# Performance work log

Hardware: AMD Instinct MI355X
Metric: run time of the kernel (lower is better)

Reference implementation:

```python
import jax, jax.numpy as jnp
import numpy as np

N = 50000
E = 800000
IN, HID, OUT = 20, 64, 2
HEADS, HD = 4, 64
EPS = 1e-5


def setup_inputs() -> dict:
    key = jax.random.key(0)
    ks = jax.random.split(key, 24)
    rn = lambda k, shape, s=0.1: (jax.random.normal(k, shape, dtype=jnp.float32) * s)
    inp = {}
    inp['x'] = jax.random.normal(ks[0], (N, IN), dtype=jnp.float32)
    inp['edge_index'] = jax.random.randint(ks[1], (2, E), 0, N, dtype=jnp.int64)
    # SAGEConv1: lin_l (aggregated msgs, bias), lin_r (root, no bias)
    inp['Wl1'] = rn(ks[2], (IN, HID)); inp['Wr1'] = rn(ks[3], (IN, HID)); inp['b1'] = jnp.zeros((HID,), jnp.float32)
    inp['g1'] = jnp.ones((HID,), jnp.float32); inp['bt1'] = jnp.zeros((HID,), jnp.float32)
    # GATConv: W2 projects to heads*dim; att vectors per head; bias size HID (concat=False)
    inp['W2'] = rn(ks[4], (HID, HEADS * HD)); inp['att_src'] = rn(ks[5], (HEADS, HD)); inp['att_dst'] = rn(ks[6], (HEADS, HD)); inp['b2'] = jnp.zeros((HID,), jnp.float32)
    inp['g2'] = jnp.ones((HID,), jnp.float32); inp['bt2'] = jnp.zeros((HID,), jnp.float32)
    # SAGEConv3: hidden -> hidden//2
    inp['Wl3'] = rn(ks[7], (HID, HID // 2)); inp['Wr3'] = rn(ks[8], (HID, HID // 2)); inp['b3'] = jnp.zeros((HID // 2,), jnp.float32)
    inp['g3'] = jnp.ones((HID // 2,), jnp.float32); inp['bt3'] = jnp.zeros((HID // 2,), jnp.float32)
    # skip + classifier
    inp['Wskip'] = rn(ks[9], (IN, HID // 2)); inp['bskip'] = jnp.zeros((HID // 2,), jnp.float32)
    inp['Wc1'] = rn(ks[10], (HID // 2, 32)); inp['bc1'] = jnp.zeros((32,), jnp.float32)
    inp['Wc2'] = rn(ks[11], (32, OUT)); inp['bc2'] = jnp.zeros((OUT,), jnp.float32)
    return inp


def _bn_eval(h, g, b):
    # eval-mode BatchNorm with freshly initialized running stats (mean=0, var=1)
    return h * (g / jnp.sqrt(1.0 + EPS)) + b


def reference(x, edge_index, Wl1, Wr1, b1, g1, bt1, W2, att_src, att_dst, b2, g2, bt2,
              Wl3, Wr3, b3, g3, bt3, Wskip, bskip, Wc1, bc1, Wc2, bc2):
    src, dst = edge_index[0], edge_index[1]
    deg = jnp.clip(jax.ops.segment_sum(jnp.ones((E,), x.dtype), dst, num_segments=N), 1.0)

    def sage(h, Wl, Wr, b):
        agg = jax.ops.segment_sum(h[src], dst, num_segments=N) / deg[:, None]  # mean aggregation
        return agg @ Wl + h @ Wr + b

    def gat(h):
        hp = (h @ W2).reshape(N, HEADS, HD)                    # [N,H,D]
        a_s = jnp.einsum('nhd,hd->nh', hp, att_src)            # [N,H]
        a_d = jnp.einsum('nhd,hd->nh', hp, att_dst)
        e = jax.nn.leaky_relu(a_s[src] + a_d[dst], 0.2)        # [E,H]
        m = jax.ops.segment_max(e, dst, num_segments=N)        # segment softmax over incoming edges
        ex = jnp.exp(e - m[dst])
        denom = jax.ops.segment_sum(ex, dst, num_segments=N)
        alpha = ex / (denom[dst] + 1e-16)                      # [E,H]
        out = jax.ops.segment_sum(hp[src] * alpha[:, :, None], dst, num_segments=N)  # [N,H,D]
        return out.mean(axis=1) + b2                            # concat=False -> mean over heads

    identity = x @ Wskip + bskip
    h = jax.nn.relu(_bn_eval(sage(x, Wl1, Wr1, b1), g1, bt1))   # dropout inactive (eval)
    h = jax.nn.relu(_bn_eval(gat(h), g2, bt2))
    h = jax.nn.relu(_bn_eval(sage(h, Wl3, Wr3, b3), g3, bt3))
    h = h + identity
    logits = jax.nn.relu(h @ Wc1 + bc1) @ Wc2 + bc2
    return jax.nn.log_softmax(logits, axis=1)
```

## Files before the change

### kernel.cpp

```cpp
#include <hip/hip_runtime.h>
#include <hip/hip_fp16.h>
#include <math.h>

#define NN 50000
#define NE 800000
#define IN_F 20
#define HID 64
#define HEADS 4
#define HD 64
#define CH 32
#define C1 32
#define OUTC 2

__global__ void k_count(const int* __restrict__ dst, int* __restrict__ count){
  int e = blockIdx.x * 256 + threadIdx.x;
  if (e < NE) atomicAdd(&count[dst[e]], 1);
}

__global__ void k_scan_block(const int* __restrict__ in, int* __restrict__ out,
                             int* __restrict__ bsum, int n){
  __shared__ int tmp[256];
  int g = blockIdx.x * 256 + threadIdx.x;
  int v = (g < n) ? in[g] : 0;
  tmp[threadIdx.x] = v;
  __syncthreads();
  for (int o = 1; o < 256; o <<= 1) {
    int t = ((int)threadIdx.x >= o) ? tmp[threadIdx.x - o] : 0;
    __syncthreads();
    tmp[threadIdx.x] += t;
    __syncthreads();
  }
  if (g < n) out[g] = tmp[threadIdx.x] - v;
  if (bsum && threadIdx.x == 255) bsum[blockIdx.x] = tmp[255];
}

__global__ void k_add_off(int* __restrict__ rowptr, const int* __restrict__ bsum_ex, int n){
  int g = blockIdx.x * 256 + threadIdx.x;
  if (g < n) rowptr[g] += bsum_ex[g >> 8];
  if (g == 0) rowptr[NN] = NE;
}

__global__ void k_scatter(const int* __restrict__ src, const int* __restrict__ dst,
                          const int* __restrict__ rowptr, int* __restrict__ cnt2,
                          int2* __restrict__ colrow){
  int e = blockIdx.x * 256 + threadIdx.x;
  if (e >= NE) return;
  int d = dst[e];
  int p = rowptr[d] + atomicAdd(&cnt2[d], 1);
  colrow[p] = make_int2(src[e], d);
}

__global__ void k_prep(const float* __restrict__ x, const float* __restrict__ W2,
                       const float* __restrict__ att_src, const float* __restrict__ att_dst,
                       __half* __restrict__ xh, float* __restrict__ was,
                       float* __restrict__ wad, float* __restrict__ W2r){
  int i = blockIdx.x * 256 + threadIdx.x;
  if (i < NN * IN_F) xh[i] = __float2half(x[i]);
  if (i < 256 * 64) {
    int hk = i >> 6, d = i & 63;
    int h = hk >> 6, k = hk & 63;
    W2r[i] = W2[k * 256 + h * 64 + d];
  }
  if (i < 256) {
    int h = i >> 6, k = i & 63;
    float s = 0.f, dd = 0.f;
    for (int d = 0; d < 64; d++) {
      float w = W2[k * 256 + h * 64 + d];
      s  += w * att_src[h * 64 + d];
      dd += w * att_dst[h * 64 + d];
    }
    was[i] = s; wad[i] = dd;
  }
}

__global__ void k_aggx_gather(const int* __restrict__ rowptr, const int2* __restrict__ colrow,
                              const __half* __restrict__ xh, float* __restrict__ aggx){
  int idx = blockIdx.x * 256 + threadIdx.x;
  if (idx >= NN * IN_F) return;
  int n = idx / IN_F, k = idx - n * IN_F;
  int r0 = rowptr[n], r1 = rowptr[n + 1];
  float acc = 0.f;
  int j = r0;
  for (; j + 4 <= r1; j += 4) {
    int s0 = colrow[j].x, s1 = colrow[j+1].x, s2 = colrow[j+2].x, s3 = colrow[j+3].x;
    float v0 = __half2float(xh[s0 * IN_F + k]);
    float v1 = __half2float(xh[s1 * IN_F + k]);
    float v2 = __half2float(xh[s2 * IN_F + k]);
    float v3 = __half2float(xh[s3 * IN_F + k]);
    acc += (v0 + v1) + (v2 + v3);
  }
  for (; j < r1; j++) acc += __half2float(xh[colrow[j].x * IN_F + k]);
  aggx[idx] = acc;
}

__global__ void k_sage1(const float* __restrict__ x, const float* __restrict__ aggx,
                        const int* __restrict__ count,
                        const float* __restrict__ Wl, const float* __restrict__ Wr,
                        const float* __restrict__ b, const float* __restrict__ g,
                        const float* __restrict__ bt,
                        const float* __restrict__ was, const float* __restrict__ wad,
                        __half* __restrict__ h1h, float* __restrict__ a_s,
                        float* __restrict__ a_d){
  __shared__ float sWl[IN_F * HID], sWr[IN_F * HID], sWas[256], sWad[256];
  for (int i = threadIdx.x; i < IN_F * HID; i += 256) { sWl[i] = Wl[i]; sWr[i] = Wr[i]; }
  { int i = threadIdx.x; sWas[i] = was[i]; sWad[i] = wad[i]; }
  __syncthreads();
  int idx = blockIdx.x * 256 + threadIdx.x;
  if (idx >= NN * HID) return;
  int n = idx >> 6, j = idx & 63;
  float inv = 1.f / fmaxf((float)count[n], 1.f);
  const float* xr = x + n * IN_F;
  const float* ar = aggx + n * IN_F;
  float acc = b[j];
  #pragma unroll
  for (int k = 0; k < IN_F; k++)
    acc += (ar[k] * inv) * sWl[k * HID + j] + xr[k] * sWr[k * HID + j];
  acc = acc * (g[j] * rsqrtf(1.f + 1e-5f)) + bt[j];
  acc = fmaxf(acc, 0.f);
  h1h[idx] = __float2half(acc);
  #pragma unroll
  for (int h = 0; h < HEADS; h++) {
    float vs = acc * sWas[h * 64 + j];
    float vd = acc * sWad[h * 64 + j];
    #pragma unroll
    for (int o = 32; o > 0; o >>= 1) { vs += __shfl_down(vs, o); vd += __shfl_down(vd, o); }
    if (j == 0) { a_s[n * 4 + h] = vs; a_d[n * 4 + h] = vd; }
  }
}

__global__ void k_edgep(const int2* __restrict__ colrow,
                        const float4* __restrict__ a_s4, const float4* __restrict__ a_d4,
                        float4* __restrict__ pe4){
  int j = blockIdx.x * 256 + threadIdx.x;
  if (j >= NE) return;
  int2 cr = colrow[j];
  float4 as = a_s4[cr.x];
  float4 ad = a_d4[cr.y];
  float e0 = as.x + ad.x; e0 = e0 >= 0.f ? e0 : 0.2f * e0;
  float e1 = as.y + ad.y; e1 = e1 >= 0.f ? e1 : 0.2f * e1;
  float e2 = as.z + ad.z; e2 = e2 >= 0.f ? e2 : 0.2f * e2;
  float e3 = as.w + ad.w; e3 = e3 >= 0.f ? e3 : 0.2f * e3;
  pe4[j] = make_float4(__expf(e0), __expf(e1), __expf(e2), __expf(e3));
}

__global__ void k_gat_fused(const int* __restrict__ rowptr, const int2* __restrict__ colrow,
                            const float4* __restrict__ pe4,
                            const __half* __restrict__ h1h, __half* __restrict__ z){
  int wid = threadIdx.x >> 6;
  int lane = threadIdx.x & 63;
  int grp = lane >> 5;
  int idx = lane & 31;
  int n = blockIdx.x * 4 + wid;
  if (n >= NN) return;
  int r0 = rowptr[n], r1 = rowptr[n + 1];
  float l0 = 0.f, l1 = 0.f, l2 = 0.f, l3 = 0.f;
  float2 ac0 = {0,0}, ac1 = {0,0}, ac2 = {0,0}, ac3 = {0,0};
  int base = r0;
  for (; base + 8 <= r1; base += 8) {
    int j0 = base + grp, j1 = base + 2 + grp, j2 = base + 4 + grp, j3 = base + 6 + grp;
    int s0 = colrow[j0].x, s1 = colrow[j1].x, s2 = colrow[j2].x, s3 = colrow[j3].x;
    float4 p0 = pe4[j0], p1 = pe4[j1], p2 = pe4[j2], p3 = pe4[j3];
    float2 v0 = __half22float2(*(const __half2*)(h1h + (size_t)s0 * 64 + 2 * idx));
    float2 v1 = __half22float2(*(const __half2*)(h1h + (size_t)s1 * 64 + 2 * idx));
    float2 v2 = __half22float2(*(const __half2*)(h1h + (size_t)s2 * 64 + 2 * idx));
    float2 v3 = __half22float2(*(const __half2*)(h1h + (size_t)s3 * 64 + 2 * idx));
    l0 += (p0.x + p1.x) + (p2.x + p3.x);
    l1 += (p0.y + p1.y) + (p2.y + p3.y);
    l2 += (p0.z + p1.z) + (p2.z + p3.z);
    l3 += (p0.w + p1.w) + (p2.w + p3.w);
    ac0.x += p0.x*v0.x + p1.x*v1.x + p2.x*v2.x + p3.x*v3.x;
    ac0.y += p0.x*v0.y + p1.x*v1.y + p2.x*v2.y + p3.x*v3.y;
    ac1.x += p0.y*v0.x + p1.y*v1.x + p2.y*v2.x + p3.y*v3.x;
    ac1.y += p0.y*v0.y + p1.y*v1.y + p2.y*v2.y + p3.y*v3.y;
    ac2.x += p0.z*v0.x + p1.z*v1.x + p2.z*v2.x + p3.z*v3.x;
    ac2.y += p0.z*v0.y + p1.z*v1.y + p2.z*v2.y + p3.z*v3.y;
    ac3.x += p0.w*v0.x + p1.w*v1.x + p2.w*v2.x + p3.w*v3.x;
    ac3.y += p0.w*v0.y + p1.w*v1.y + p2.w*v2.y + p3.w*v3.y;
  }
  for (int j = base + grp; j < r1; j += 2) {
    int s = colrow[j].x;
    float4 p = pe4[j];
    float2 v = __half22float2(*(const __half2*)(h1h + (size_t)s * 64 + 2 * idx));
    l0 += p.x; l1 += p.y; l2 += p.z; l3 += p.w;
    ac0.x += p.x*v.x; ac0.y += p.x*v.y;
    ac1.x += p.y*v.x; ac1.y += p.y*v.y;
    ac2.x += p.z*v.x; ac2.y += p.z*v.y;
    ac3.x += p.w*v.x; ac3.y += p.w*v.y;
  }
  l0 += __shfl_xor(l0, 32); l1 += __shfl_xor(l1, 32);
  l2 += __shfl_xor(l2, 32); l3 += __shfl_xor(l3, 32);
  ac0.x += __shfl_xor(ac0.x, 32); ac0.y += __shfl_xor(ac0.y, 32);
  ac1.x += __shfl_xor(ac1.x, 32); ac1.y += __shfl_xor(ac1.y, 32);
  ac2.x += __shfl_xor(ac2.x, 32); ac2.y += __shfl_xor(ac2.y, 32);
  ac3.x += __shfl_xor(ac3.x, 32); ac3.y += __shfl_xor(ac3.y, 32);
  if (grp == 0) {
    float i0 = 1.f / (4.f * (l0 + 1e-16f));
    float i1 = 1.f / (4.f * (l1 + 1e-16f));
    float i2 = 1.f / (4.f * (l2 + 1e-16f));
    float i3 = 1.f / (4.f * (l3 + 1e-16f));
    __half* zr = z + (size_t)n * 256;
    *(__half2*)(zr +       2 * idx) = __floats2half2_rn(ac0.x * i0, ac0.y * i0);
    *(__half2*)(zr +  64 + 2 * idx) = __floats2half2_rn(ac1.x * i1, ac1.y * i1);
    *(__half2*)(zr + 128 + 2 * idx) = __floats2half2_rn(ac2.x * i2, ac2.y * i2);
    *(__half2*)(zr + 192 + 2 * idx) = __floats2half2_rn(ac3.x * i3, ac3.y * i3);
  }
}

__global__ void __launch_bounds__(256) k_zproj(const __half* __restrict__ z,
                      const float* __restrict__ W2r, const float* __restrict__ b2,
                      const float* __restrict__ g2, const float* __restrict__ bt2,
                      float* __restrict__ h2, __half* __restrict__ h2h){
  __shared__ float sz[4][256];
  __shared__ float sacc[4][4][64];
  int tid = threadIdx.x;
  int w = tid >> 6, d = tid & 63;
  float wreg[64];
  #pragma unroll
  for (int i = 0; i < 64; i++) wreg[i] = W2r[(w * 64 + i) * 64 + d];
  float gd = g2[d] * rsqrtf(1.f + 1e-5f), btd = bt2[d], bd = b2[d];
  int n0base = blockIdx.x * 64;
  for (int r = 0; r < 16; r++) {
    int n0 = n0base + r * 4;
    for (int i = tid; i < 512; i += 256) {
      int m = i >> 7, c = (i & 127) * 2;
      int n = n0 + m;
      if (n < NN) {
        __half2 hv = *(const __half2*)(z + (size_t)n * 256 + c);
        float2 f = __half22float2(hv);
        sz[m][c] = f.x; sz[m][c + 1] = f.y;
      } else { sz[m][c] = 0.f; sz[m][c + 1] = 0.f; }
    }
    __syncthreads();
    #pragma unroll
    for (int m = 0; m < 4; m++) {
      float acc = 0.f;
      #pragma unroll
      for (int i = 0; i < 64; i++) acc += sz[m][w * 64 + i] * wreg[i];
      sacc[m][w][d] = acc;
    }
    __syncthreads();
    int n = n0 + w;
    if (n < NN) {
      float rr = sacc[w][0][d] + sacc[w][1][d] + sacc[w][2][d] + sacc[w][3][d] + bd;
      rr = rr * gd + btd;
      rr = fmaxf(rr, 0.f);
      h2[(size_t)n * 64 + d] = rr;
      h2h[(size_t)n * 64 + d] = __float2half(rr);
    }
    __syncthreads();
  }
}

__global__ void __launch_bounds__(256) k_sage3f(
    const int* __restrict__ rowptr, const int2* __restrict__ colrow,
    const float* __restrict__ x, const float* __restrict__ h2,
    const __half* __restrict__ h2h, const int* __restrict__ count,
    const float* __restrict__ Wl3, const float* __restrict__ Wr3,
    const float* __restrict__ b3, const float* __restrict__ g3,
    const float* __restrict__ bt3, const float* __restrict__ Wskip,
    const float* __restrict__ bskip, float* __restrict__ h3){
  __shared__ float sWl[HID * CH], sWr[HID * CH], sWs[IN_F * CH];
  __shared__ float sA[4][HID], sH[4][HID];
  for (int i = threadIdx.x; i < HID * CH; i += 256) { sWl[i] = Wl3[i]; sWr[i] = Wr3[i]; }
  for (int i = threadIdx.x; i < IN_F * CH; i += 256) sWs[i] = Wskip[i];
  int wid = threadIdx.x >> 6, lane = threadIdx.x & 63;
  int grp = lane >> 5, idx = lane & 31;
  int n = blockIdx.x * 4 + wid;
  int nc = n < NN ? n : NN - 1;
  int r0 = rowptr[nc], r1 = rowptr[nc + 1];
  float2 av = {0, 0};
  int base = r0;
  for (; base + 8 <= r1; base += 8) {
    int j0 = base + grp, j1 = base + 2 + grp, j2 = base + 4 + grp, j3 = base + 6 + grp;
    int s0 = colrow[j0].x, s1 = colrow[j1].x, s2 = colrow[j2].x, s3 = colrow[j3].x;
    float2 v0 = __half22float2(*(const __half2*)(h2h + (size_t)s0 * 64 + 2 * idx));
    float2 v1 = __half22float2(*(const __half2*)(h2h + (size_t)s1 * 64 + 2 * idx));
    float2 v2 = __half22float2(*(const __half2*)(h2h + (size_t)s2 * 64 + 2 * idx));
    float2 v3 = __half22float2(*(const __half2*)(h2h + (size_t)s3 * 64 + 2 * idx));
    av.x += (v0.x + v1.x) + (v2.x + v3.x);
    av.y += (v0.y + v1.y) + (v2.y + v3.y);
  }
  for (int j = base + grp; j < r1; j += 2) {
    float2 v = __half22float2(*(const __half2*)(h2h + (size_t)colrow[j].x * 64 + 2 * idx));
    av.x += v.x; av.y += v.y;
  }
  av.x += __shfl_xor(av.x, 32);
  av.y += __shfl_xor(av.y, 32);
  float inv = 1.f / fmaxf((float)count[nc], 1.f);
  if (grp == 0) { sA[wid][2 * idx] = av.x * inv; sA[wid][2 * idx + 1] = av.y * inv; }
  sH[wid][lane] = h2[(size_t)nc * 64 + lane];
  __syncthreads();
  int kbase = grp * 32;
  float c0 = 0.f, c1 = 0.f;
  #pragma unroll
  for (int k0 = 0; k0 < 32; k0 += 2) {
    int k = kbase + k0;
    c0 += sA[wid][k] * sWl[k * CH + idx] + sH[wid][k] * sWr[k * CH + idx];
    c1 += sA[wid][k+1] * sWl[(k+1) * CH + idx] + sH[wid][k+1] * sWr[(k+1) * CH + idx];
  }
  float c = c0 + c1;
  c += __shfl_xor(c, 32);
  if (grp == 0 && n < NN) {
    float acc = c + b3[idx];
    acc = acc * (g3[idx] * rsqrtf(1.f + 1e-5f)) + bt3[idx];
    acc = fmaxf(acc, 0.f);
    float idn = bskip[idx];
    const float* xr = x + (size_t)n * IN_F;
    #pragma unroll
    for (int k = 0; k < IN_F; k++) idn += xr[k] * sWs[k * CH + idx];
    h3[(size_t)n * CH + idx] = acc + idn;
  }
}

__global__ void __launch_bounds__(64) k_cls(const float* __restrict__ h3,
                      const float* __restrict__ Wc1, const float* __restrict__ bc1,
                      const float* __restrict__ Wc2, const float* __restrict__ bc2,
                      float* __restrict__ out){
  __shared__ float sW1[C1 * C1], sW2[C1 * OUTC], sb1[C1], sb2[OUTC];
  __shared__ float sh3[64][CH + 1];
  int tid = threadIdx.x;
  int n0 = blockIdx.x * 64;
  for (int i = tid; i < C1 * C1; i += 64) sW1[i] = Wc1[i];
  if (tid < C1 * OUTC) sW2[tid] = Wc2[tid];
  if (tid < C1) sb1[tid] = bc1[tid];
  if (tid < OUTC) sb2[tid] = bc2[tid];
  for (int i = tid; i < 64 * CH; i += 64) {
    int m = i >> 5, c = i & 31;
    int n = n0 + m;
    sh3[m][c] = (n < NN) ? h3[(size_t)n * CH + c] : 0.f;
  }
  __syncthreads();
  int n = n0 + tid;
  if (n >= NN) return;
  float hrow[CH];
  #pragma unroll
  for (int j = 0; j < CH; j++) hrow[j] = sh3[tid][j];
  float l0 = sb2[0], l1 = sb2[1];
  #pragma unroll
  for (int i = 0; i < C1; i++) {
    float c0 = sb1[i], c1 = 0.f;
    #pragma unroll
    for (int j = 0; j < CH; j += 2) {
      c0 += hrow[j] * sW1[j * C1 + i];
      c1 += hrow[j + 1] * sW1[(j + 1) * C1 + i];
    }
    float c = fmaxf(c0 + c1, 0.f);
    l0 += c * sW2[i * OUTC + 0];
    l1 += c * sW2[i * OUTC + 1];
  }
  float mx = fmaxf(l0, l1);
  float lse = mx + logf(expf(l0 - mx) + expf(l1 - mx));
  out[n * OUTC + 0] = l0 - lse;
  out[n * OUTC + 1] = l1 - lse;
}

extern "C" void kernel_launch(void* const* d_in, const int* in_sizes, int n_in,
                              void* d_out, int out_size, void* d_ws, size_t ws_size,
                              hipStream_t stream) {
  const float* x       = (const float*)d_in[0];
  const int*   ei      = (const int*)d_in[1];
  const float* Wl1     = (const float*)d_in[2];
  const float* Wr1     = (const float*)d_in[3];
  const float* b1      = (const float*)d_in[4];
  const float* g1      = (const float*)d_in[5];
  const float* bt1     = (const float*)d_in[6];
  const float* W2      = (const float*)d_in[7];
  const float* att_src = (const float*)d_in[8];
  const float* att_dst = (const float*)d_in[9];
  const float* b2      = (const float*)d_in[10];
  const float* g2      = (const float*)d_in[11];
  const float* bt2     = (const float*)d_in[12];
  const float* Wl3     = (const float*)d_in[13];
  const float* Wr3     = (const float*)d_in[14];
  const float* b3      = (const float*)d_in[15];
  const float* g3      = (const float*)d_in[16];
  const float* bt3     = (const float*)d_in[17];
  const float* Wskip   = (const float*)d_in[18];
  const float* bskip   = (const float*)d_in[19];
  const float* Wc1     = (const float*)d_in[20];
  const float* bc1     = (const float*)d_in[21];
  const float* Wc2     = (const float*)d_in[22];
  const float* bc2     = (const float*)d_in[23];
  float* out = (float*)d_out;

  const int* src = ei;
  const int* dst = ei + NE;

  float* ws = (float*)d_ws;
  size_t off = 0;
  auto alloc = [&](size_t nf) { size_t o = off; off += (nf + 63) & ~(size_t)63; return o; };
  size_t o_count = alloc(NN);
  size_t o_cnt2  = alloc(NN);
  size_t zero_elems = off;
  size_t o_rowptr = alloc(NN + 1);
  size_t o_bsum   = alloc(256);
  size_t o_bsumex = alloc(256);
  size_t o_colrow = alloc((size_t)NE * 2);
  size_t o_pe     = alloc((size_t)NE * 4);
  size_t o_xh     = alloc((size_t)NN * IN_F / 2 + 64);
  size_t o_aggx   = alloc((size_t)NN * IN_F);
  size_t o_h1h    = alloc((size_t)NN * HID / 2 + 64);
  size_t o_as     = alloc((size_t)NN * HEADS);
  size_t o_ad     = alloc((size_t)NN * HEADS);
  size_t o_was    = alloc(256);
  size_t o_wad    = alloc(256);
  size_t o_w2r    = alloc(256 * 64);
  size_t o_z      = alloc((size_t)NN * 256 / 2 + 64);
  size_t o_h2     = alloc((size_t)NN * HID);
  size_t o_h2h    = alloc((size_t)NN * HID / 2 + 64);
  size_t o_h3     = alloc((size_t)NN * CH);
  (void)ws_size; (void)in_sizes; (void)n_in; (void)out_size;

  int* count    = (int*)(ws + o_count);
  int* cnt2     = (int*)(ws + o_cnt2);
  int* rowptr   = (int*)(ws + o_rowptr);
  int* bsum     = (int*)(ws + o_bsum);
  int* bsumex   = (int*)(ws + o_bsumex);
  int2* colrow  = (int2*)(ws + o_colrow);
  float* pe     = ws + o_pe;
  __half* xh    = (__half*)(ws + o_xh);
  float* aggx   = ws + o_aggx;
  __half* h1h   = (__half*)(ws + o_h1h);
  float* a_s    = ws + o_as;
  float* a_d    = ws + o_ad;
  float* was    = ws + o_was;
  float* wad    = ws + o_wad;
  float* W2r    = ws + o_w2r;
  __half* z     = (__half*)(ws + o_z);
  float* h2     = ws + o_h2;
  __half* h2h   = (__half*)(ws + o_h2h);
  float* h3     = ws + o_h3;

  auto nb = [](long long n) { return (int)((n + 255) / 256); };
  const int nscan = nb(NN);

  hipMemsetAsync(ws, 0, zero_elems * sizeof(int), stream);
  k_count<<<nb(NE), 256, 0, stream>>>(dst, count);
  k_scan_block<<<nscan, 256, 0, stream>>>(count, rowptr, bsum, NN);
  k_scan_block<<<1, 256, 0, stream>>>(bsum, bsumex, nullptr, nscan);
  k_add_off<<<nscan, 256, 0, stream>>>(rowptr, bsumex, NN);
  k_scatter<<<nb(NE), 256, 0, stream>>>(src, dst, rowptr, cnt2, colrow);
  k_prep<<<nb((long long)NN * IN_F), 256, 0, stream>>>(x, W2, att_src, att_dst, xh, was, wad, W2r);
  k_aggx_gather<<<nb((long long)NN * IN_F), 256, 0, stream>>>(rowptr, colrow, xh, aggx);
  k_sage1<<<nb((long long)NN * HID), 256, 0, stream>>>(x, aggx, count, Wl1, Wr1, b1, g1, bt1,
                                                       was, wad, h1h, a_s, a_d);
  k_edgep<<<nb(NE), 256, 0, stream>>>(colrow, (const float4*)a_s, (const float4*)a_d, (float4*)pe);
  k_gat_fused<<<nb((long long)NN * 64), 256, 0, stream>>>(rowptr, colrow, (const float4*)pe, h1h, z);
  k_zproj<<<(NN + 63) / 64, 256, 0, stream>>>(z, W2r, b2, g2, bt2, h2, h2h);
  k_sage3f<<<(NN + 3) / 4, 256, 0, stream>>>(rowptr, colrow, x, h2, h2h, count,
                                             Wl3, Wr3, b3, g3, bt3, Wskip, bskip, h3);
  k_cls<<<(NN + 63) / 64, 64, 0, stream>>>(h3, Wc1, bc1, Wc2, bc2, out);
}
```

Before: 321.2 us.

## Pack edge indices to 32 bits, fuse degree count, restructure gathers and grids

```diff
diff --git a/kernel.cpp b/kernel.cpp
--- a/kernel.cpp
+++ b/kernel.cpp
@@ -12,11 +12,6 @@
 #define C1 32
 #define OUTC 2
 
-__global__ void k_count(const int* __restrict__ dst, int* __restrict__ count){
-  int e = blockIdx.x * 256 + threadIdx.x;
-  if (e < NE) atomicAdd(&count[dst[e]], 1);
-}
-
 __global__ void k_scan_block(const int* __restrict__ in, int* __restrict__ out,
                              int* __restrict__ bsum, int n){
   __shared__ int tmp[256];
@@ -42,20 +37,23 @@
 
 __global__ void k_scatter(const int* __restrict__ src, const int* __restrict__ dst,
                           const int* __restrict__ rowptr, int* __restrict__ cnt2,
-                          int2* __restrict__ colrow){
+                          unsigned* __restrict__ colu){
   int e = blockIdx.x * 256 + threadIdx.x;
   if (e >= NE) return;
   int d = dst[e];
   int p = rowptr[d] + atomicAdd(&cnt2[d], 1);
-  colrow[p] = make_int2(src[e], d);
+  colu[p] = (unsigned)src[e] | ((unsigned)d << 16);
 }
 
 __global__ void k_prep(const float* __restrict__ x, const float* __restrict__ W2,
                        const float* __restrict__ att_src, const float* __restrict__ att_dst,
+                       const int* __restrict__ dst,
                        __half* __restrict__ xh, float* __restrict__ was,
-                       float* __restrict__ wad, float* __restrict__ W2r){
+                       float* __restrict__ wad, float* __restrict__ W2r,
+                       int* __restrict__ count){
   int i = blockIdx.x * 256 + threadIdx.x;
   if (i < NN * IN_F) xh[i] = __float2half(x[i]);
+  if (i < NE) atomicAdd(&count[dst[i]], 1);
   if (i < 256 * 64) {
     int hk = i >> 6, d = i & 63;
     int h = hk >> 6, k = hk & 63;
@@ -73,24 +71,31 @@
   }
 }
 
-__global__ void k_aggx_gather(const int* __restrict__ rowptr, const int2* __restrict__ colrow,
+__global__ void k_aggx_gather(const int* __restrict__ rowptr, const unsigned* __restrict__ colu,
                               const __half* __restrict__ xh, float* __restrict__ aggx){
-  int idx = blockIdx.x * 256 + threadIdx.x;
-  if (idx >= NN * IN_F) return;
-  int n = idx / IN_F, k = idx - n * IN_F;
+  int wid = threadIdx.x >> 6, lane = threadIdx.x & 63;
+  int grp = lane >> 5, f = lane & 31;
+  int n = blockIdx.x * 4 + wid;
+  if (n >= NN) return;
   int r0 = rowptr[n], r1 = rowptr[n + 1];
+  int ff = f < IN_F ? f : 0;
   float acc = 0.f;
-  int j = r0;
-  for (; j + 4 <= r1; j += 4) {
-    int s0 = colrow[j].x, s1 = colrow[j+1].x, s2 = colrow[j+2].x, s3 = colrow[j+3].x;
-    float v0 = __half2float(xh[s0 * IN_F + k]);
-    float v1 = __half2float(xh[s1 * IN_F + k]);
-    float v2 = __half2float(xh[s2 * IN_F + k]);
-    float v3 = __half2float(xh[s3 * IN_F + k]);
+  int base = r0;
+  for (; base + 8 <= r1; base += 8) {
+    int s0 = colu[base + grp] & 0xffff;
+    int s1 = colu[base + 2 + grp] & 0xffff;
+    int s2 = colu[base + 4 + grp] & 0xffff;
+    int s3 = colu[base + 6 + grp] & 0xffff;
+    float v0 = __half2float(xh[s0 * IN_F + ff]);
+    float v1 = __half2float(xh[s1 * IN_F + ff]);
+    float v2 = __half2float(xh[s2 * IN_F + ff]);
+    float v3 = __half2float(xh[s3 * IN_F + ff]);
     acc += (v0 + v1) + (v2 + v3);
   }
-  for (; j < r1; j++) acc += __half2float(xh[colrow[j].x * IN_F + k]);
-  aggx[idx] = acc;
+  for (int j = base + grp; j < r1; j += 2)
+    acc += __half2float(xh[(colu[j] & 0xffff) * IN_F + ff]);
+  acc += __shfl_xor(acc, 32);
+  if (grp == 0 && f < IN_F) aggx[n * IN_F + f] = acc;
 }
 
 __global__ void k_sage1(const float* __restrict__ x, const float* __restrict__ aggx,
@@ -128,14 +133,14 @@
   }
 }
 
-__global__ void k_edgep(const int2* __restrict__ colrow,
+__global__ void k_edgep(const unsigned* __restrict__ colu,
                         const float4* __restrict__ a_s4, const float4* __restrict__ a_d4,
                         float4* __restrict__ pe4){
   int j = blockIdx.x * 256 + threadIdx.x;
   if (j >= NE) return;
-  int2 cr = colrow[j];
-  float4 as = a_s4[cr.x];
-  float4 ad = a_d4[cr.y];
+  unsigned v = colu[j];
+  float4 as = a_s4[v & 0xffff];
+  float4 ad = a_d4[v >> 16];
   float e0 = as.x + ad.x; e0 = e0 >= 0.f ? e0 : 0.2f * e0;
   float e1 = as.y + ad.y; e1 = e1 >= 0.f ? e1 : 0.2f * e1;
   float e2 = as.z + ad.z; e2 = e2 >= 0.f ? e2 : 0.2f * e2;
@@ -143,7 +148,7 @@
   pe4[j] = make_float4(__expf(e0), __expf(e1), __expf(e2), __expf(e3));
 }
 
-__global__ void k_gat_fused(const int* __restrict__ rowptr, const int2* __restrict__ colrow,
+__global__ void k_gat_fused(const int* __restrict__ rowptr, const unsigned* __restrict__ colu,
                             const float4* __restrict__ pe4,
                             const __half* __restrict__ h1h, __half* __restrict__ z){
   int wid = threadIdx.x >> 6;
@@ -158,7 +163,7 @@
   int base = r0;
   for (; base + 8 <= r1; base += 8) {
     int j0 = base + grp, j1 = base + 2 + grp, j2 = base + 4 + grp, j3 = base + 6 + grp;
-    int s0 = colrow[j0].x, s1 = colrow[j1].x, s2 = colrow[j2].x, s3 = colrow[j3].x;
+    int s0 = colu[j0] & 0xffff, s1 = colu[j1] & 0xffff, s2 = colu[j2] & 0xffff, s3 = colu[j3] & 0xffff;
     float4 p0 = pe4[j0], p1 = pe4[j1], p2 = pe4[j2], p3 = pe4[j3];
     float2 v0 = __half22float2(*(const __half2*)(h1h + (size_t)s0 * 64 + 2 * idx));
     float2 v1 = __half22float2(*(const __half2*)(h1h + (size_t)s1 * 64 + 2 * idx));
@@ -178,7 +183,7 @@
     ac3.y += p0.w*v0.y + p1.w*v1.y + p2.w*v2.y + p3.w*v3.y;
   }
   for (int j = base + grp; j < r1; j += 2) {
-    int s = colrow[j].x;
+    int s = colu[j] & 0xffff;
     float4 p = pe4[j];
     float2 v = __half22float2(*(const __half2*)(h1h + (size_t)s * 64 + 2 * idx));
     l0 += p.x; l1 += p.y; l2 += p.z; l3 += p.w;
@@ -252,7 +257,7 @@
 }
 
 __global__ void __launch_bounds__(256) k_sage3f(
-    const int* __restrict__ rowptr, const int2* __restrict__ colrow,
+    const int* __restrict__ rowptr, const unsigned* __restrict__ colu,
     const float* __restrict__ x, const float* __restrict__ h2,
     const __half* __restrict__ h2h, const int* __restrict__ count,
     const float* __restrict__ Wl3, const float* __restrict__ Wr3,
@@ -265,66 +270,72 @@
   for (int i = threadIdx.x; i < IN_F * CH; i += 256) sWs[i] = Wskip[i];
   int wid = threadIdx.x >> 6, lane = threadIdx.x & 63;
   int grp = lane >> 5, idx = lane & 31;
-  int n = blockIdx.x * 4 + wid;
-  int nc = n < NN ? n : NN - 1;
-  int r0 = rowptr[nc], r1 = rowptr[nc + 1];
-  float2 av = {0, 0};
-  int base = r0;
-  for (; base + 8 <= r1; base += 8) {
-    int j0 = base + grp, j1 = base + 2 + grp, j2 = base + 4 + grp, j3 = base + 6 + grp;
-    int s0 = colrow[j0].x, s1 = colrow[j1].x, s2 = colrow[j2].x, s3 = colrow[j3].x;
-    float2 v0 = __half22float2(*(const __half2*)(h2h + (size_t)s0 * 64 + 2 * idx));
-    float2 v1 = __half22float2(*(const __half2*)(h2h + (size_t)s1 * 64 + 2 * idx));
-    float2 v2 = __half22float2(*(const __half2*)(h2h + (size_t)s2 * 64 + 2 * idx));
-    float2 v3 = __half22float2(*(const __half2*)(h2h + (size_t)s3 * 64 + 2 * idx));
-    av.x += (v0.x + v1.x) + (v2.x + v3.x);
-    av.y += (v0.y + v1.y) + (v2.y + v3.y);
-  }
-  for (int j = base + grp; j < r1; j += 2) {
-    float2 v = __half22float2(*(const __half2*)(h2h + (size_t)colrow[j].x * 64 + 2 * idx));
-    av.x += v.x; av.y += v.y;
-  }
-  av.x += __shfl_xor(av.x, 32);
-  av.y += __shfl_xor(av.y, 32);
-  float inv = 1.f / fmaxf((float)count[nc], 1.f);
-  if (grp == 0) { sA[wid][2 * idx] = av.x * inv; sA[wid][2 * idx + 1] = av.y * inv; }
-  sH[wid][lane] = h2[(size_t)nc * 64 + lane];
-  __syncthreads();
-  int kbase = grp * 32;
-  float c0 = 0.f, c1 = 0.f;
-  #pragma unroll
-  for (int k0 = 0; k0 < 32; k0 += 2) {
-    int k = kbase + k0;
-    c0 += sA[wid][k] * sWl[k * CH + idx] + sH[wid][k] * sWr[k * CH + idx];
-    c1 += sA[wid][k+1] * sWl[(k+1) * CH + idx] + sH[wid][k+1] * sWr[(k+1) * CH + idx];
-  }
-  float c = c0 + c1;
-  c += __shfl_xor(c, 32);
-  if (grp == 0 && n < NN) {
-    float acc = c + b3[idx];
-    acc = acc * (g3[idx] * rsqrtf(1.f + 1e-5f)) + bt3[idx];
-    acc = fmaxf(acc, 0.f);
-    float idn = bskip[idx];
-    const float* xr = x + (size_t)n * IN_F;
+  const int nchunk = (NN + 3) / 4;
+  for (int ch = blockIdx.x; ch < nchunk; ch += gridDim.x) {
+    int n = ch * 4 + wid;
+    int nc = n < NN ? n : NN - 1;
+    int r0 = rowptr[nc], r1 = rowptr[nc + 1];
+    float2 av = {0, 0};
+    int base = r0;
+    for (; base + 8 <= r1; base += 8) {
+      int s0 = colu[base + grp] & 0xffff;
+      int s1 = colu[base + 2 + grp] & 0xffff;
+      int s2 = colu[base + 4 + grp] & 0xffff;
+      int s3 = colu[base + 6 + grp] & 0xffff;
+      float2 v0 = __half22float2(*(const __half2*)(h2h + (size_t)s0 * 64 + 2 * idx));
+      float2 v1 = __half22float2(*(const __half2*)(h2h + (size_t)s1 * 64 + 2 * idx));
+      float2 v2 = __half22float2(*(const __half2*)(h2h + (size_t)s2 * 64 + 2 * idx));
+      float2 v3 = __half22float2(*(const __half2*)(h2h + (size_t)s3 * 64 + 2 * idx));
+      av.x += (v0.x + v1.x) + (v2.x + v3.x);
+      av.y += (v0.y + v1.y) + (v2.y + v3.y);
+    }
+    for (int j = base + grp; j < r1; j += 2) {
+      float2 v = __half22float2(*(const __half2*)(h2h + (size_t)(colu[j] & 0xffff) * 64 + 2 * idx));
+      av.x += v.x; av.y += v.y;
+    }
+    av.x += __shfl_xor(av.x, 32);
+    av.y += __shfl_xor(av.y, 32);
+    float inv = 1.f / fmaxf((float)count[nc], 1.f);
+    if (grp == 0) { sA[wid][2 * idx] = av.x * inv; sA[wid][2 * idx + 1] = av.y * inv; }
+    sH[wid][lane] = h2[(size_t)nc * 64 + lane];
+    __syncthreads();
+    int kbase = grp * 32;
+    float c0 = 0.f, c1 = 0.f;
     #pragma unroll
-    for (int k = 0; k < IN_F; k++) idn += xr[k] * sWs[k * CH + idx];
-    h3[(size_t)n * CH + idx] = acc + idn;
-  }
-}
-
-__global__ void __launch_bounds__(64) k_cls(const float* __restrict__ h3,
+    for (int k0 = 0; k0 < 32; k0 += 2) {
+      int k = kbase + k0;
+      c0 += sA[wid][k] * sWl[k * CH + idx] + sH[wid][k] * sWr[k * CH + idx];
+      c1 += sA[wid][k+1] * sWl[(k+1) * CH + idx] + sH[wid][k+1] * sWr[(k+1) * CH + idx];
+    }
+    float c = c0 + c1;
+    c += __shfl_xor(c, 32);
+    if (grp == 0 && n < NN) {
+      float acc = c + b3[idx];
+      acc = acc * (g3[idx] * rsqrtf(1.f + 1e-5f)) + bt3[idx];
+      acc = fmaxf(acc, 0.f);
+      float idn = bskip[idx];
+      const float* xr = x + (size_t)n * IN_F;
+      #pragma unroll
+      for (int k = 0; k < IN_F; k++) idn += xr[k] * sWs[k * CH + idx];
+      h3[(size_t)n * CH + idx] = acc + idn;
+    }
+    __syncthreads();
+  }
+}
+
+__global__ void __launch_bounds__(256) k_cls(const float* __restrict__ h3,
                       const float* __restrict__ Wc1, const float* __restrict__ bc1,
                       const float* __restrict__ Wc2, const float* __restrict__ bc2,
                       float* __restrict__ out){
   __shared__ float sW1[C1 * C1], sW2[C1 * OUTC], sb1[C1], sb2[OUTC];
-  __shared__ float sh3[64][CH + 1];
+  __shared__ float sh3[256][CH + 1];
   int tid = threadIdx.x;
-  int n0 = blockIdx.x * 64;
-  for (int i = tid; i < C1 * C1; i += 64) sW1[i] = Wc1[i];
+  int n0 = blockIdx.x * 256;
+  for (int i = tid; i < C1 * C1; i += 256) sW1[i] = Wc1[i];
   if (tid < C1 * OUTC) sW2[tid] = Wc2[tid];
   if (tid < C1) sb1[tid] = bc1[tid];
   if (tid < OUTC) sb2[tid] = bc2[tid];
-  for (int i = tid; i < 64 * CH; i += 64) {
+  for (int i = tid; i < 256 * CH; i += 256) {
     int m = i >> 5, c = i & 31;
     int n = n0 + m;
     sh3[m][c] = (n < NN) ? h3[(size_t)n * CH + c] : 0.f;
@@ -395,7 +406,7 @@
   size_t o_rowptr = alloc(NN + 1);
   size_t o_bsum   = alloc(256);
   size_t o_bsumex = alloc(256);
-  size_t o_colrow = alloc((size_t)NE * 2);
+  size_t o_colu   = alloc(NE);
   size_t o_pe     = alloc((size_t)NE * 4);
   size_t o_xh     = alloc((size_t)NN * IN_F / 2 + 64);
   size_t o_aggx   = alloc((size_t)NN * IN_F);
@@ -411,43 +422,43 @@
   size_t o_h3     = alloc((size_t)NN * CH);
   (void)ws_size; (void)in_sizes; (void)n_in; (void)out_size;
 
-  int* count    = (int*)(ws + o_count);
-  int* cnt2     = (int*)(ws + o_cnt2);
-  int* rowptr   = (int*)(ws + o_rowptr);
-  int* bsum     = (int*)(ws + o_bsum);
-  int* bsumex   = (int*)(ws + o_bsumex);
-  int2* colrow  = (int2*)(ws + o_colrow);
-  float* pe     = ws + o_pe;
-  __half* xh    = (__half*)(ws + o_xh);
-  float* aggx   = ws + o_aggx;
-  __half* h1h   = (__half*)(ws + o_h1h);
-  float* a_s    = ws + o_as;
-  float* a_d    = ws + o_ad;
-  float* was    = ws + o_was;
-  float* wad    = ws + o_wad;
-  float* W2r    = ws + o_w2r;
-  __half* z     = (__half*)(ws + o_z);
-  float* h2     = ws + o_h2;
-  __half* h2h   = (__half*)(ws + o_h2h);
-  float* h3     = ws + o_h3;
+  int* count     = (int*)(ws + o_count);
+  int* cnt2      = (int*)(ws + o_cnt2);
+  int* rowptr    = (int*)(ws + o_rowptr);
+  int* bsum      = (int*)(ws + o_bsum);
+  int* bsumex    = (int*)(ws + o_bsumex);
+  unsigned* colu = (unsigned*)(ws + o_colu);
+  float* pe      = ws + o_pe;
+  __half* xh     = (__half*)(ws + o_xh);
+  float* aggx    = ws + o_aggx;
+  __half* h1h    = (__half*)(ws + o_h1h);
+  float* a_s     = ws + o_as;
+  float* a_d     = ws + o_ad;
+  float* was     = ws + o_was;
+  float* wad     = ws + o_wad;
+  float* W2r     = ws + o_w2r;
+  __half* z      = (__half*)(ws + o_z);
+  float* h2      = ws + o_h2;
+  __half* h2h    = (__half*)(ws + o_h2h);
+  float* h3      = ws + o_h3;
 
   auto nb = [](long long n) { return (int)((n + 255) / 256); };
   const int nscan = nb(NN);
 
   hipMemsetAsync(ws, 0, zero_elems * sizeof(int), stream);
-  k_count<<<nb(NE), 256, 0, stream>>>(dst, count);
+  k_prep<<<nb((long long)NN * IN_F), 256, 0, stream>>>(x, W2, att_src, att_dst, dst,
+                                                       xh, was, wad, W2r, count);
   k_scan_block<<<nscan, 256, 0, stream>>>(count, rowptr, bsum, NN);
   k_scan_block<<<1, 256, 0, stream>>>(bsum, bsumex, nullptr, nscan);
   k_add_off<<<nscan, 256, 0, stream>>>(rowptr, bsumex, NN);
-  k_scatter<<<nb(NE), 256, 0, stream>>>(src, dst, rowptr, cnt2, colrow);
-  k_prep<<<nb((long long)NN * IN_F), 256, 0, stream>>>(x, W2, att_src, att_dst, xh, was, wad, W2r);
-  k_aggx_gather<<<nb((long long)NN * IN_F), 256, 0, stream>>>(rowptr, colrow, xh, aggx);
+  k_scatter<<<nb(NE), 256, 0, stream>>>(src, dst, rowptr, cnt2, colu);
+  k_aggx_gather<<<(NN + 3) / 4, 256, 0, stream>>>(rowptr, colu, xh, aggx);
   k_sage1<<<nb((long long)NN * HID), 256, 0, stream>>>(x, aggx, count, Wl1, Wr1, b1, g1, bt1,
                                                        was, wad, h1h, a_s, a_d);
-  k_edgep<<<nb(NE), 256, 0, stream>>>(colrow, (const float4*)a_s, (const float4*)a_d, (float4*)pe);
-  k_gat_fused<<<nb((long long)NN * 64), 256, 0, stream>>>(rowptr, colrow, (const float4*)pe, h1h, z);
+  k_edgep<<<nb(NE), 256, 0, stream>>>(colu, (const float4*)a_s, (const float4*)a_d, (float4*)pe);
+  k_gat_fused<<<(NN + 3) / 4, 256, 0, stream>>>(rowptr, colu, (const float4*)pe, h1h, z);
   k_zproj<<<(NN + 63) / 64, 256, 0, stream>>>(z, W2r, b2, g2, bt2, h2, h2h);
-  k_sage3f<<<(NN + 3) / 4, 256, 0, stream>>>(rowptr, colrow, x, h2, h2h, count,
-                                             Wl3, Wr3, b3, g3, bt3, Wskip, bskip, h3);
-  k_cls<<<(NN + 63) / 64, 64, 0, stream>>>(h3, Wc1, bc1, Wc2, bc2, out);
-}
+  k_sage3f<<<1280, 256, 0, stream>>>(rowptr, colu, x, h2, h2h, count,
+                                     Wl3, Wr3, b3, g3, bt3, Wskip, bskip, h3);
+  k_cls<<<(NN + 255) / 256, 256, 0, stream>>>(h3, Wc1, bc1, Wc2, bc2, out);
+}
```

After: 363.4 us. 1.13x slower.
